# Optimization experiments

Hardware: AMD Instinct MI355X
Metric: run time of the kernel (lower is better)

The kernel has to match this reference:

```python
import jax, jax.numpy as jnp
import numpy as np

B, S, D, H = 2, 2048, 768, 12
E = D // H  # d_head = 64


def setup_inputs() -> dict:
    key = jax.random.key(0)
    ks = jax.random.split(key, 10)
    scale = 1.0 / np.sqrt(D)
    x = jax.random.normal(ks[0], (B, S, D), dtype=jnp.float32)
    # Additive mask, laid out [H*B, S, S] as the torch forward slices per head.
    attn_mask = jnp.zeros((H * B, S, S), dtype=jnp.float32)
    # Per-head projections (math form: q = x @ Wq[h] + bq[h])
    Wq = jax.random.normal(ks[1], (H, D, E), dtype=jnp.float32) * scale
    bq = jax.random.normal(ks[2], (H, E), dtype=jnp.float32) * 0.01
    Wk = jax.random.normal(ks[3], (H, D, E), dtype=jnp.float32) * scale
    bk = jax.random.normal(ks[4], (H, E), dtype=jnp.float32) * 0.01
    Wv = jax.random.normal(ks[5], (H, D, E), dtype=jnp.float32) * scale
    bv = jax.random.normal(ks[6], (H, E), dtype=jnp.float32) * 0.01
    Wo = jax.random.normal(ks[7], (D, D), dtype=jnp.float32) * scale
    bo = jax.random.normal(ks[8], (D,), dtype=jnp.float32) * 0.01
    return {"x": x, "attn_mask": attn_mask, "Wq": Wq, "bq": bq,
            "Wk": Wk, "bk": bk, "Wv": Wv, "bv": bv, "Wo": Wo, "bo": bo}


def reference(x, attn_mask, Wq, bq, Wk, bk, Wv, bv, Wo, bo):
    # x: [B,S,D]; attn_mask: [H*B,S,S]
    q = jnp.einsum('bsd,hde->hbse', x, Wq) + bq[:, None, None, :]
    k = jnp.einsum('bsd,hde->hbse', x, Wk) + bk[:, None, None, :]
    v = jnp.einsum('bsd,hde->hbse', x, Wv) + bv[:, None, None, :]
    mask = attn_mask.reshape(H, B, S, S)
    # NOTE: original code has NO 1/sqrt(d_head) scaling — kept faithful.
    logits = jnp.einsum('hbse,hbte->hbst', q, k) + mask
    w = jax.nn.softmax(logits, axis=-1)  # dropout is identity at eval / p=0
    o = jnp.einsum('hbst,hbte->hbse', w, v)  # [H,B,S,E]
    o = jnp.transpose(o, (1, 2, 0, 3)).reshape(B, S, H * E)  # concat heads
    return o @ Wo + bo
```

## Files before the change

kernel.cpp:

```cpp
#include <hip/hip_runtime.h>
#include <hip/hip_bf16.h>
#include <cmath>

constexpr int Bc  = 2;
constexpr int Sc  = 2048;
constexpr int Dc  = 768;
constexpr int Hc  = 12;
constexpr int Ec  = 64;
constexpr int BSc = Bc * Sc;

typedef _Float16 f16;
typedef __attribute__((ext_vector_type(8)))  _Float16 half8;
typedef __attribute__((ext_vector_type(16))) float    floatx16;

typedef __attribute__((address_space(3))) void       lds_void;
typedef __attribute__((address_space(1))) const void glb_cvoid;


__global__ __launch_bounds__(256) void prep_kernel(
    const float* __restrict__ x,
    const float* __restrict__ Wq, const float* __restrict__ Wk, const float* __restrict__ Wv,
    const float* __restrict__ bq, const float* __restrict__ bk, const float* __restrict__ bv,
    const float* __restrict__ Wo,
    f16* __restrict__ x16, f16* __restrict__ Wt16, f16* __restrict__ Wot16,
    float* __restrict__ bias_cat)
{
    __shared__ __align__(16) float Ts[64][65];
    const int t = threadIdx.x;
    int bid = blockIdx.x;

    if (bid < 1536) {
        const size_t base = (size_t)bid * 2048 + t * 8;
        const float4 v0 = *(const float4*)(x + base);
        const float4 v1 = *(const float4*)(x + base + 4);
        half8 hv;
        hv[0] = (f16)v0.x; hv[1] = (f16)v0.y; hv[2] = (f16)v0.z; hv[3] = (f16)v0.w;
        hv[4] = (f16)v1.x; hv[5] = (f16)v1.y; hv[6] = (f16)v1.z; hv[7] = (f16)v1.w;
        *(half8*)(x16 + base) = hv;
        return;
    }
    bid -= 1536;
    if (bid < 432) {
        const int proj = bid / 144, rem = bid % 144, h = rem / 12, dt = rem % 12;
        const float* W = ((proj == 0) ? Wq : (proj == 1) ? Wk : Wv) + (size_t)h * Dc * Ec;
        const int c = t & 63, rr = t >> 6;
        #pragma unroll
        for (int r0 = 0; r0 < 64; r0 += 4) {
            const int d = rr + r0;
            Ts[d][c] = W[(size_t)(dt * 64 + d) * Ec + c];
        }
        __syncthreads();
        #pragma unroll
        for (int r0 = 0; r0 < 64; r0 += 4) {
            const int e = rr + r0;
            Wt16[(size_t)(proj * 768 + h * 64 + e) * Dc + dt * 64 + c] = (f16)Ts[c][e];
        }
        return;
    }
    bid -= 432;
    if (bid < 144) {
        const int rt = bid / 12, ct = bid % 12;
        const int c = t & 63, rr = t >> 6;
        #pragma unroll
        for (int r0 = 0; r0 < 64; r0 += 4) {
            const int d = rr + r0;
            Ts[d][c] = Wo[(size_t)(rt * 64 + d) * Dc + ct * 64 + c];
        }
        __syncthreads();
        #pragma unroll
        for (int r0 = 0; r0 < 64; r0 += 4) {
            const int e = rr + r0;
            Wot16[(size_t)(ct * 64 + e) * Dc + rt * 64 + c] = (f16)Ts[c][e];
        }
        return;
    }
    bid -= 144;
    {
        const int g = bid * 256 + t;
        if (g < 3 * 768) {
            const int proj = g / 768, idx = g % 768;
            const float* bb = (proj == 0) ? bq : (proj == 1) ? bk : bv;
            bias_cat[g] = bb[idx];
        }
    }
}

__global__ __launch_bounds__(256, 2) void gemm_qkv_kernel(
    const f16* __restrict__ x16, const f16* __restrict__ Wt16,
    const float* __restrict__ bias_cat,
    f16* __restrict__ q16, f16* __restrict__ kswz, f16* __restrict__ vswz)
{
    __shared__ __align__(16) unsigned char smem[34816];
    f16 (*As)[64]  = (f16(*)[64])smem;
    f16 (*Bs)[64]  = (f16(*)[64])(smem + 16384);
    f16 (*Cs)[136] = (f16(*)[136])smem;

    const int t = threadIdx.x;
    const int wave = t >> 6, lane = t & 63;
    const int col = lane & 31, hf = lane >> 5;
    const int wr = wave & 1, wc = wave >> 1;
    const int m0 = blockIdx.x * 128, n0 = blockIdx.y * 128;
    const int lrow = lane >> 3, lseg = lane & 7;

    floatx16 c00, c01, c10, c11;
    #pragma unroll
    for (int i = 0; i < 16; ++i) { c00[i] = 0.f; c01[i] = 0.f; c10[i] = 0.f; c11[i] = 0.f; }

    for (int k0 = 0; k0 < Dc; k0 += 64) {
        #pragma unroll
        for (int i = 0; i < 4; ++i) {
            const int r = wave * 32 + i * 8;
            __builtin_amdgcn_global_load_lds(
                (glb_cvoid*)(x16 + (size_t)(m0 + r + lrow) * Dc + k0 + lseg * 8),
                (lds_void*)&As[r][0], 16, 0, 0);
            __builtin_amdgcn_global_load_lds(
                (glb_cvoid*)(Wt16 + (size_t)(n0 + r + lrow) * Dc + k0 + lseg * 8),
                (lds_void*)&Bs[r][0], 16, 0, 0);
        }
        __syncthreads();
        #pragma unroll
        for (int ks = 0; ks < 4; ++ks) {
            const half8 a0 = *(const half8*)&As[wr * 64 + col][ks * 16 + hf * 8];
            const half8 a1 = *(const half8*)&As[wr * 64 + 32 + col][ks * 16 + hf * 8];
            const half8 b0 = *(const half8*)&Bs[wc * 64 + col][ks * 16 + hf * 8];
            const half8 b1 = *(const half8*)&Bs[wc * 64 + 32 + col][ks * 16 + hf * 8];
            c00 = __builtin_amdgcn_mfma_f32_32x32x16_f16(a0, b0, c00, 0, 0, 0);
            c01 = __builtin_amdgcn_mfma_f32_32x32x16_f16(a0, b1, c01, 0, 0, 0);
            c10 = __builtin_amdgcn_mfma_f32_32x32x16_f16(a1, b0, c10, 0, 0, 0);
            c11 = __builtin_amdgcn_mfma_f32_32x32x16_f16(a1, b1, c11, 0, 0, 0);
        }
        __syncthreads();
    }

    const float bias0 = bias_cat[n0 + wc * 64 + col];
    const float bias1 = bias_cat[n0 + wc * 64 + 32 + col];
    #pragma unroll
    for (int i = 0; i < 16; ++i) {
        const int r = (i & 3) + 8 * (i >> 2) + 4 * hf;
        Cs[wr * 64 + r][wc * 64 + col]           = (f16)(c00[i] + bias0);
        Cs[wr * 64 + r][wc * 64 + 32 + col]      = (f16)(c01[i] + bias1);
        Cs[wr * 64 + 32 + r][wc * 64 + col]      = (f16)(c10[i] + bias0);
        Cs[wr * 64 + 32 + r][wc * 64 + 32 + col] = (f16)(c11[i] + bias1);
    }
    __syncthreads();

    const int proj = n0 / 768;
    const int h0   = (n0 - proj * 768) >> 6;
    const int b    = m0 >> 11;
    const int s_in = m0 & 2047;
    const int kt0  = s_in >> 5;

    if (proj == 0) {
        const int row = t >> 1, seg = t & 1;
        const int h = h0 + seg;
        f16* gp = q16 + ((size_t)(h * Bc + b) * Sc + s_in + row) * Ec;
        #pragma unroll
        for (int j = 0; j < 8; ++j)
            *(half8*)(gp + j * 8) = *(const half8*)&Cs[row][seg * 64 + j * 8];
    } else if (proj == 1) {
        #pragma unroll
        for (int ch = 0; ch < 8; ++ch) {
            const int id = ch * 256 + t;
            const int lane_ = id & 63;
            const int ks  = (id >> 6) & 3;
            const int ktp = (id >> 8) & 3;
            const int seg = (id >> 10) & 1;
            const int colp = lane_ & 31, hfp = lane_ >> 5;
            const int hb = (h0 + seg) * Bc + b;
            const half8 val = *(const half8*)&Cs[ktp * 32 + colp][seg * 64 + ks * 16 + hfp * 8];
            *(half8*)(kswz + ((size_t)((hb * 64 + kt0 + ktp) * 4 + ks) << 9) + lane_ * 8) = val;
        }
    } else {
        #pragma unroll
        for (int ch = 0; ch < 8; ++ch) {
            const int id = ch * 256 + t;
            const int lane_ = id & 63;
            const int ks2 = (id >> 6) & 1;
            const int vh  = (id >> 7) & 1;
            const int ktp = (id >> 8) & 3;
            const int seg = (id >> 10) & 1;
            const int colp = lane_ & 31, hfp = lane_ >> 5;
            const int hb = (h0 + seg) * Bc + b;
            const int e  = vh * 32 + colp;
            half8 val;
            #pragma unroll
            for (int j = 0; j < 8; ++j)
                val[j] = Cs[ktp * 32 + ks2 * 16 + hfp * 8 + j][seg * 64 + e];
            *(half8*)(vswz + ((size_t)(((hb * 64 + kt0 + ktp) * 2 + ks2) * 2 + vh) << 9) + lane_ * 8) = val;
        }
    }
}

__global__ __launch_bounds__(256, 2) void flash_attn_kernel(
    const f16* __restrict__ q16, const f16* __restrict__ kswz,
    const f16* __restrict__ vswz, const float* __restrict__ mask,
    f16* __restrict__ obuf16)
{
    __shared__ _Float16 Plds[4][32][40];
    __shared__ float Msh[2][2][32];
    __shared__ float Lsh[2][32];
    __shared__ float OLsh[2][64][33];

    const int rb   = blockIdx.x;
    const int b    = blockIdx.y;
    const int h    = blockIdx.z;
    const int hb   = h * Bc + b;
    const int t    = threadIdx.x;
    const int wave = t >> 6;
    const int lane = t & 63;
    const int rg   = wave & 1;
    const int kh   = wave >> 1;
    const int col  = lane & 31;
    const int hf   = lane >> 5;
    const int row0 = rb * 64 + rg * 32;

    const f16* qb  = q16  + ((size_t)hb * Sc + row0) * Ec;
    const f16* kbz = kswz + ((size_t)hb << 17);
    const f16* vbz = vswz + ((size_t)hb << 17);

    half8 qfrag[4];
    #pragma unroll
    for (int ks = 0; ks < 4; ++ks)
        qfrag[ks] = *(const half8*)(qb + (size_t)col * Ec + ks * 16 + hf * 8);

    constexpr int NT = (Sc / 2) / 32;

    float vmax[16];
    #pragma unroll
    for (int i = 0; i < 16; ++i) vmax[i] = -3e38f;

    half8 kreg[4];
    {
        const f16* kp = kbz + ((size_t)(kh * NT) << 11) + lane * 8;
        #pragma unroll
        for (int ks = 0; ks < 4; ++ks) kreg[ks] = *(const half8*)(kp + (ks << 9));
    }
    #pragma unroll 2
    for (int kt = 0; kt < NT; ++kt) {
        floatx16 c;
        #pragma unroll
        for (int i = 0; i < 16; ++i) c[i] = 0.f;
        #pragma unroll
        for (int ks = 0; ks < 4; ++ks)
            c = __builtin_amdgcn_mfma_f32_32x32x16_f16(qfrag[ks], kreg[ks], c, 0, 0, 0);
        if (kt + 1 < NT) {
            const f16* kp = kbz + ((size_t)(kh * NT + kt + 1) << 11) + lane * 8;
            #pragma unroll
            for (int ks = 0; ks < 4; ++ks) kreg[ks] = *(const half8*)(kp + (ks << 9));
        }
        #pragma unroll
        for (int i = 0; i < 16; ++i) vmax[i] = fmaxf(vmax[i], c[i]);
    }
    #pragma unroll
    for (int i = 0; i < 16; ++i) {
        float v = vmax[i];
        v = fmaxf(v, __shfl_xor(v, 1));
        v = fmaxf(v, __shfl_xor(v, 2));
        v = fmaxf(v, __shfl_xor(v, 4));
        v = fmaxf(v, __shfl_xor(v, 8));
        v = fmaxf(v, __shfl_xor(v, 16));
        vmax[i] = v;
    }
    if (col == 0) {
        #pragma unroll
        for (int i = 0; i < 16; ++i) {
            const int r = (i & 3) + 8 * (i >> 2) + 4 * hf;
            Msh[kh][rg][r] = vmax[i];
        }
    }
    __syncthreads();
    float mrow[16];
    #pragma unroll
    for (int i = 0; i < 16; ++i) {
        const int r = (i & 3) + 8 * (i >> 2) + 4 * hf;
        mrow[i] = fmaxf(vmax[i], Msh[1 - kh][rg][r]);
    }

    floatx16 o0, o1;
    float lsum[16];
    #pragma unroll
    for (int i = 0; i < 16; ++i) { o0[i] = 0.f; o1[i] = 0.f; lsum[i] = 0.f; }

    const float* mbase = mask + ((size_t)hb * Sc + row0) * Sc + col;
    const int key_base = kh * (Sc / 2);

    float mb[4][16];
    #pragma unroll
    for (int d = 0; d < 4; ++d)
        #pragma unroll
        for (int i = 0; i < 16; ++i) {
            const int r = (i & 3) + 8 * (i >> 2) + 4 * hf;
            mb[d][i] = __builtin_nontemporal_load(
                mbase + (size_t)r * Sc + key_base + d * 32);
        }
    {
        const f16* kp = kbz + ((size_t)(kh * NT) << 11) + lane * 8;
        #pragma unroll
        for (int ks = 0; ks < 4; ++ks) kreg[ks] = *(const half8*)(kp + (ks << 9));
    }

    for (int kt4 = 0; kt4 < NT; kt4 += 4) {
        #pragma unroll
        for (int s = 0; s < 4; ++s) {
            const int kt  = kt4 + s;
            const int ktg = kh * NT + kt;

            const f16* vp = vbz + ((size_t)ktg << 11) + lane * 8;
            const half8 va  = *(const half8*)(vp);
            const half8 vb0 = *(const half8*)(vp + (1 << 9));
            const half8 vc  = *(const half8*)(vp + (2 << 9));
            const half8 vd  = *(const half8*)(vp + (3 << 9));

            floatx16 c;
            #pragma unroll
            for (int i = 0; i < 16; ++i) c[i] = 0.f;
            #pragma unroll
            for (int ks = 0; ks < 4; ++ks)
                c = __builtin_amdgcn_mfma_f32_32x32x16_f16(qfrag[ks], kreg[ks], c, 0, 0, 0);

            if (kt + 1 < NT) {
                const f16* kp = kbz + ((size_t)(ktg + 1) << 11) + lane * 8;
                #pragma unroll
                for (int ks = 0; ks < 4; ++ks) kreg[ks] = *(const half8*)(kp + (ks << 9));
            }

            #pragma unroll
            for (int i = 0; i < 16; ++i) {
                const float p = __expf(c[i] + mb[s][i] - mrow[i]);
                lsum[i] += p;
                const int r = (i & 3) + 8 * (i >> 2) + 4 * hf;
                Plds[wave][r][col] = (f16)p;
            }
            if (kt4 + s + 4 < NT) {
                #pragma unroll
                for (int i = 0; i < 16; ++i) {
                    const int r = (i & 3) + 8 * (i >> 2) + 4 * hf;
                    mb[s][i] = __builtin_nontemporal_load(
                        mbase + (size_t)r * Sc + key_base + (kt + 4) * 32);
                }
            }
            asm volatile("s_waitcnt lgkmcnt(0)" ::: "memory");

            #pragma unroll
            for (int ks2 = 0; ks2 < 2; ++ks2) {
                const half8 pf = *(const half8*)(&Plds[wave][col][ks2 * 16 + hf * 8]);
                const half8 v0 = (ks2 == 0) ? va : vc;
                const half8 v1 = (ks2 == 0) ? vb0 : vd;
                o0 = __builtin_amdgcn_mfma_f32_32x32x16_f16(pf, v0, o0, 0, 0, 0);
                o1 = __builtin_amdgcn_mfma_f32_32x32x16_f16(pf, v1, o1, 0, 0, 0);
            }
        }
    }

    #pragma unroll
    for (int i = 0; i < 16; ++i) {
        float v = lsum[i];
        v += __shfl_xor(v, 1);
        v += __shfl_xor(v, 2);
        v += __shfl_xor(v, 4);
        v += __shfl_xor(v, 8);
        v += __shfl_xor(v, 16);
        lsum[i] = v;
    }

    if (kh == 1) {
        if (col == 0) {
            #pragma unroll
            for (int i = 0; i < 16; ++i) {
                const int r = (i & 3) + 8 * (i >> 2) + 4 * hf;
                Lsh[rg][r] = lsum[i];
            }
        }
        #pragma unroll
        for (int i = 0; i < 16; ++i) {
            OLsh[rg][lane][i]      = o0[i];
            OLsh[rg][lane][16 + i] = o1[i];
        }
    }
    __syncthreads();
    if (kh == 0) {
        #pragma unroll
        for (int i = 0; i < 16; ++i) {
            const int r = (i & 3) + 8 * (i >> 2) + 4 * hf;
            const float inv = 1.f / (lsum[i] + Lsh[rg][r]);
            const float r0 = (o0[i] + OLsh[rg][lane][i])      * inv;
            const float r1 = (o1[i] + OLsh[rg][lane][16 + i]) * inv;
            const size_t orow = ((size_t)b * Sc + row0 + r) * Dc + h * Ec;
            obuf16[orow + col]      = (f16)r0;
            obuf16[orow + 32 + col] = (f16)r1;
        }
    }
}

__global__ __launch_bounds__(256, 2) void gemm_out_kernel(
    const f16* __restrict__ a16, const f16* __restrict__ Wot16,
    const float* __restrict__ bo, float* __restrict__ out)
{
    __shared__ __align__(16) f16 As[128][64];
    __shared__ __align__(16) f16 Bs[64][64];

    const int t = threadIdx.x;
    const int wave = t >> 6, lane = t & 63;
    const int col = lane & 31, hf = lane >> 5;
    const int m0 = blockIdx.x * 128, n0 = blockIdx.y * 64;
    const int lrow = lane >> 3, lseg = lane & 7;

    floatx16 c0, c1;
    #pragma unroll
    for (int i = 0; i < 16; ++i) { c0[i] = 0.f; c1[i] = 0.f; }

    for (int k0 = 0; k0 < Dc; k0 += 64) {
        #pragma unroll
        for (int i = 0; i < 4; ++i) {
            const int r = wave * 32 + i * 8;
            __builtin_amdgcn_global_load_lds(
                (glb_cvoid*)(a16 + (size_t)(m0 + r + lrow) * Dc + k0 + lseg * 8),
                (lds_void*)&As[r][0], 16, 0, 0);
        }
        {
            const int r = wave * 16;
            __builtin_amdgcn_global_load_lds(
                (glb_cvoid*)(Wot16 + (size_t)(n0 + r + lrow) * Dc + k0 + lseg * 8),
                (lds_void*)&Bs[r][0], 16, 0, 0);
            __builtin_amdgcn_global_load_lds(
                (glb_cvoid*)(Wot16 + (size_t)(n0 + r + 8 + lrow) * Dc + k0 + lseg * 8),
                (lds_void*)&Bs[r + 8][0], 16, 0, 0);
        }
        __syncthreads();
        #pragma unroll
        for (int ks = 0; ks < 4; ++ks) {
            const half8 a  = *(const half8*)&As[wave * 32 + col][ks * 16 + hf * 8];
            const half8 b0 = *(const half8*)&Bs[col][ks * 16 + hf * 8];
            const half8 b1 = *(const half8*)&Bs[32 + col][ks * 16 + hf * 8];
            c0 = __builtin_amdgcn_mfma_f32_32x32x16_f16(a, b0, c0, 0, 0, 0);
            c1 = __builtin_amdgcn_mfma_f32_32x32x16_f16(a, b1, c1, 0, 0, 0);
        }
        __syncthreads();
    }

    const float bo0 = bo[n0 + col], bo1 = bo[n0 + 32 + col];
    #pragma unroll
    for (int i = 0; i < 16; ++i) {
        const int r = (i & 3) + 8 * (i >> 2) + 4 * hf;
        const size_t ro = (size_t)(m0 + wave * 32 + r) * Dc + n0;
        out[ro + col]      = c0[i] + bo0;
        out[ro + 32 + col] = c1[i] + bo1;
    }
}

extern "C" void kernel_launch(void* const* d_in, const int* in_sizes, int n_in,
                              void* d_out, int out_size, void* d_ws, size_t ws_size,
                              hipStream_t stream)
{
    const float* x    = (const float*)d_in[0];
    const float* mask = (const float*)d_in[1];
    const float* Wq   = (const float*)d_in[2];
    const float* bq   = (const float*)d_in[3];
    const float* Wk   = (const float*)d_in[4];
    const float* bk   = (const float*)d_in[5];
    const float* Wv   = (const float*)d_in[6];
    const float* bv   = (const float*)d_in[7];
    const float* Wo   = (const float*)d_in[8];
    const float* bo   = (const float*)d_in[9];
    float* out = (float*)d_out;

    constexpr size_t NQ = (size_t)Hc * Bc * Sc * Ec;
    f16* x16    = (f16*)d_ws;
    f16* Wt16   = x16 + (size_t)BSc * Dc;
    f16* Wot16  = Wt16 + (size_t)3 * Dc * Dc;
    f16* q16    = Wot16 + (size_t)Dc * Dc;
    f16* kswz   = q16 + NQ;
    f16* vswz   = kswz + NQ;
    f16* obuf16 = vswz + NQ;
    float* bias_cat = (float*)(obuf16 + NQ);

    prep_kernel<<<2121, 256, 0, stream>>>(x, Wq, Wk, Wv, bq, bk, bv, Wo,
                                          x16, Wt16, Wot16, bias_cat);

    gemm_qkv_kernel<<<dim3(BSc / 128, 2304 / 128), 256, 0, stream>>>(
        x16, Wt16, bias_cat, q16, kswz, vswz);

    flash_attn_kernel<<<dim3(Sc / 64, Bc, Hc), 256, 0, stream>>>(
        q16, kswz, vswz, mask, obuf16);

    gemm_out_kernel<<<dim3(BSc / 128, Dc / 64), 256, 0, stream>>>(
        obuf16, Wot16, bo, out);
}
```

Baseline: 677.9 us.

## Stage attention mask through LDS with coalesced float4 loads and remap block order

The mask is now read with row-coalesced float4 nontemporal loads, double-buffered in registers, and written to a per-wave LDS tile. The softmax reads it from that tile, replacing the previous scattered per-element global loads that were held in a large 64-float register array. Shared memory is overlaid into a single blob (mask tiles alias the output-reduction buffer), so a barrier is added before the reduction. The launch bound rises to 3 blocks per CU, and a 1D grid remaps blocks so that 8 head-batch pairs are interleaved. The cost is extra LDS traffic and tighter register limits.

```diff
diff --git a/kernel.cpp b/kernel.cpp
--- a/kernel.cpp
+++ b/kernel.cpp
@@ -12,6 +12,7 @@
 typedef _Float16 f16;
 typedef __attribute__((ext_vector_type(8)))  _Float16 half8;
 typedef __attribute__((ext_vector_type(16))) float    floatx16;
+typedef __attribute__((ext_vector_type(4)))  float    fx4;
 
 typedef __attribute__((address_space(3))) void       lds_void;
 typedef __attribute__((address_space(1))) const void glb_cvoid;
@@ -191,20 +192,25 @@
     }
 }
 
-__global__ __launch_bounds__(256, 2) void flash_attn_kernel(
+__global__ __launch_bounds__(256, 3) void flash_attn_kernel(
     const f16* __restrict__ q16, const f16* __restrict__ kswz,
     const f16* __restrict__ vswz, const float* __restrict__ mask,
     f16* __restrict__ obuf16)
 {
-    __shared__ _Float16 Plds[4][32][40];
-    __shared__ float Msh[2][2][32];
-    __shared__ float Lsh[2][32];
-    __shared__ float OLsh[2][64][33];
-
-    const int rb   = blockIdx.x;
-    const int b    = blockIdx.y;
-    const int h    = blockIdx.z;
-    const int hb   = h * Bc + b;
+    __shared__ __align__(16) unsigned char shblob[10240 + 16896 + 512 + 256];
+    _Float16 (*Plds)[32][40] = (_Float16(*)[32][40])shblob;
+    float*    Mall           = (float*)(shblob + 10240);
+    float    (*OLsh)[64][33] = (float(*)[64][33])(shblob + 10240);
+    float    (*Msh)[2][32]   = (float(*)[2][32])(shblob + 10240 + 16896);
+    float    (*Lsh)[32]      = (float(*)[32])(shblob + 10240 + 16896 + 512);
+
+    const int fblk = blockIdx.x;
+    const int kk   = fblk >> 3;
+    const int hb   = (fblk & 7) + 8 * (kk >> 5);
+    const int rb   = kk & 31;
+    const int h    = hb >> 1;
+    const int b    = hb & 1;
+
     const int t    = threadIdx.x;
     const int wave = t >> 6;
     const int lane = t & 63;
@@ -213,6 +219,8 @@
     const int col  = lane & 31;
     const int hf   = lane >> 5;
     const int row0 = rb * 64 + rg * 32;
+    const int lrow8 = lane >> 3;
+    const int lcol4 = (lane & 7) * 4;
 
     const f16* qb  = q16  + ((size_t)hb * Sc + row0) * Ec;
     const f16* kbz = kswz + ((size_t)hb << 17);
@@ -281,74 +289,78 @@
     #pragma unroll
     for (int i = 0; i < 16; ++i) { o0[i] = 0.f; o1[i] = 0.f; lsum[i] = 0.f; }
 
-    const float* mbase = mask + ((size_t)hb * Sc + row0) * Sc + col;
+    const float* mw = mask + ((size_t)hb * Sc + row0) * Sc;
     const int key_base = kh * (Sc / 2);
-
-    float mb[4][16];
-    #pragma unroll
-    for (int d = 0; d < 4; ++d)
+    float* Mw = Mall + wave * 1024;
+
+    fx4 mreg[4];
+    #pragma unroll
+    for (int j = 0; j < 4; ++j)
+        mreg[j] = __builtin_nontemporal_load(
+            (const fx4*)(mw + (size_t)(j * 8 + lrow8) * Sc + key_base + lcol4));
+    #pragma unroll
+    for (int j = 0; j < 4; ++j)
+        *(fx4*)&Mw[(j * 8 + lrow8) * 32 + lcol4] = mreg[j];
+    #pragma unroll
+    for (int j = 0; j < 4; ++j)
+        mreg[j] = __builtin_nontemporal_load(
+            (const fx4*)(mw + (size_t)(j * 8 + lrow8) * Sc + key_base + 32 + lcol4));
+    {
+        const f16* kp = kbz + ((size_t)(kh * NT) << 11) + lane * 8;
+        #pragma unroll
+        for (int ks = 0; ks < 4; ++ks) kreg[ks] = *(const half8*)(kp + (ks << 9));
+    }
+
+    for (int kt = 0; kt < NT; ++kt) {
+        const int ktg = kh * NT + kt;
+
+        const f16* vp = vbz + ((size_t)ktg << 11) + lane * 8;
+        const half8 va  = *(const half8*)(vp);
+        const half8 vb0 = *(const half8*)(vp + (1 << 9));
+        const half8 vc  = *(const half8*)(vp + (2 << 9));
+        const half8 vd  = *(const half8*)(vp + (3 << 9));
+
+        floatx16 c;
+        #pragma unroll
+        for (int i = 0; i < 16; ++i) c[i] = 0.f;
+        #pragma unroll
+        for (int ks = 0; ks < 4; ++ks)
+            c = __builtin_amdgcn_mfma_f32_32x32x16_f16(qfrag[ks], kreg[ks], c, 0, 0, 0);
+
+        if (kt + 1 < NT) {
+            const f16* kp = kbz + ((size_t)(ktg + 1) << 11) + lane * 8;
+            #pragma unroll
+            for (int ks = 0; ks < 4; ++ks) kreg[ks] = *(const half8*)(kp + (ks << 9));
+        }
+
         #pragma unroll
         for (int i = 0; i < 16; ++i) {
             const int r = (i & 3) + 8 * (i >> 2) + 4 * hf;
-            mb[d][i] = __builtin_nontemporal_load(
-                mbase + (size_t)r * Sc + key_base + d * 32);
-        }
-    {
-        const f16* kp = kbz + ((size_t)(kh * NT) << 11) + lane * 8;
-        #pragma unroll
-        for (int ks = 0; ks < 4; ++ks) kreg[ks] = *(const half8*)(kp + (ks << 9));
-    }
-
-    for (int kt4 = 0; kt4 < NT; kt4 += 4) {
-        #pragma unroll
-        for (int s = 0; s < 4; ++s) {
-            const int kt  = kt4 + s;
-            const int ktg = kh * NT + kt;
-
-            const f16* vp = vbz + ((size_t)ktg << 11) + lane * 8;
-            const half8 va  = *(const half8*)(vp);
-            const half8 vb0 = *(const half8*)(vp + (1 << 9));
-            const half8 vc  = *(const half8*)(vp + (2 << 9));
-            const half8 vd  = *(const half8*)(vp + (3 << 9));
-
-            floatx16 c;
+            const float p = __expf(c[i] + Mw[r * 32 + col] - mrow[i]);
+            lsum[i] += p;
+            Plds[wave][r][col] = (f16)p;
+        }
+        if (kt + 1 < NT) {
             #pragma unroll
-            for (int i = 0; i < 16; ++i) c[i] = 0.f;
+            for (int j = 0; j < 4; ++j)
+                *(fx4*)&Mw[(j * 8 + lrow8) * 32 + lcol4] = mreg[j];
+        }
+        if (kt + 2 < NT) {
             #pragma unroll
-            for (int ks = 0; ks < 4; ++ks)
-                c = __builtin_amdgcn_mfma_f32_32x32x16_f16(qfrag[ks], kreg[ks], c, 0, 0, 0);
-
-            if (kt + 1 < NT) {
-                const f16* kp = kbz + ((size_t)(ktg + 1) << 11) + lane * 8;
-                #pragma unroll
-                for (int ks = 0; ks < 4; ++ks) kreg[ks] = *(const half8*)(kp + (ks << 9));
-            }
-
-            #pragma unroll
-            for (int i = 0; i < 16; ++i) {
-                const float p = __expf(c[i] + mb[s][i] - mrow[i]);
-                lsum[i] += p;
-                const int r = (i & 3) + 8 * (i >> 2) + 4 * hf;
-                Plds[wave][r][col] = (f16)p;
-            }
-            if (kt4 + s + 4 < NT) {
-                #pragma unroll
-                for (int i = 0; i < 16; ++i) {
-                    const int r = (i & 3) + 8 * (i >> 2) + 4 * hf;
-                    mb[s][i] = __builtin_nontemporal_load(
-                        mbase + (size_t)r * Sc + key_base + (kt + 4) * 32);
-                }
-            }
-            asm volatile("s_waitcnt lgkmcnt(0)" ::: "memory");
-
-            #pragma unroll
-            for (int ks2 = 0; ks2 < 2; ++ks2) {
-                const half8 pf = *(const half8*)(&Plds[wave][col][ks2 * 16 + hf * 8]);
-                const half8 v0 = (ks2 == 0) ? va : vc;
-                const half8 v1 = (ks2 == 0) ? vb0 : vd;
-                o0 = __builtin_amdgcn_mfma_f32_32x32x16_f16(pf, v0, o0, 0, 0, 0);
-                o1 = __builtin_amdgcn_mfma_f32_32x32x16_f16(pf, v1, o1, 0, 0, 0);
-            }
+            for (int j = 0; j < 4; ++j)
+                mreg[j] = __builtin_nontemporal_load(
+                    (const fx4*)(mw + (size_t)(j * 8 + lrow8) * Sc
+                                 + key_base + (kt + 2) * 32 + lcol4));
+        }
+        asm volatile("s_waitcnt lgkmcnt(0)" ::: "memory");
+
+        #pragma unroll
+        for (int ks2 = 0; ks2 < 2; ++ks2) {
+            const half8 pf = *(const half8*)(&Plds[wave][col][ks2 * 16 + hf * 8]);
+            const half8 v0 = (ks2 == 0) ? va : vc;
+            const half8 v1 = (ks2 == 0) ? vb0 : vd;
+            o0 = __builtin_amdgcn_mfma_f32_32x32x16_f16(pf, v0, o0, 0, 0, 0);
+            o1 = __builtin_amdgcn_mfma_f32_32x32x16_f16(pf, v1, o1, 0, 0, 0);
         }
     }
 
@@ -363,6 +375,7 @@
         lsum[i] = v;
     }
 
+    __syncthreads();
     if (kh == 1) {
         if (col == 0) {
             #pragma unroll
@@ -480,7 +493,7 @@
     gemm_qkv_kernel<<<dim3(BSc / 128, 2304 / 128), 256, 0, stream>>>(
         x16, Wt16, bias_cat, q16, kswz, vswz);
 
-    flash_attn_kernel<<<dim3(Sc / 64, Bc, Hc), 256, 0, stream>>>(
+    flash_attn_kernel<<<768, 256, 0, stream>>>(
         q16, kswz, vswz, mask, obuf16);
 
     gemm_out_kernel<<<dim3(BSc / 128, Dc / 64), 256, 0, stream>>>(
```

Measured after the change: 665.3 us. No clear change (-1.9%).

## Stage mask tiles into LDS via async loads and drop key-split waves

Applied to the files above, without the earlier changes.

The attention kernel now uses 128-thread blocks of two waves. Each wave owns 32 query rows and loops over all keys, which removes the key-half split and its cross-wave max/sum/output merge through shared memory. The additive mask is now loaded per 64x128 band with global_load_lds directly into a 32KB LDS buffer, replacing the per-lane nontemporal register prefetch. A flattened grid remaps blocks so neighbouring blocks share heads. This lowers register pressure and coalesces the mask reads, but adds two barriers per round with no double-buffering, so mask load latency is exposed, and each wave now runs twice as many serial iterations.

```diff
diff --git a/kernel.cpp b/kernel.cpp
--- a/kernel.cpp
+++ b/kernel.cpp
@@ -191,39 +191,39 @@
     }
 }
 
-__global__ __launch_bounds__(256, 2) void flash_attn_kernel(
+__global__ __launch_bounds__(128, 2) void flash_attn_kernel(
     const f16* __restrict__ q16, const f16* __restrict__ kswz,
     const f16* __restrict__ vswz, const float* __restrict__ mask,
     f16* __restrict__ obuf16)
 {
-    __shared__ _Float16 Plds[4][32][40];
-    __shared__ float Msh[2][2][32];
-    __shared__ float Lsh[2][32];
-    __shared__ float OLsh[2][64][33];
-
-    const int rb   = blockIdx.x;
-    const int b    = blockIdx.y;
-    const int h    = blockIdx.z;
-    const int hb   = h * Bc + b;
+    __shared__ __align__(16) float Mall[64 * 128];
+    __shared__ _Float16 Plds[2][32][40];
+
+    const int fblk = blockIdx.x;
+    const int kk   = fblk >> 3;
+    const int hb   = (fblk & 7) + 8 * (kk >> 5);
+    const int rb   = kk & 31;
+    const int h    = hb >> 1;
+    const int b    = hb & 1;
+
     const int t    = threadIdx.x;
     const int wave = t >> 6;
     const int lane = t & 63;
-    const int rg   = wave & 1;
-    const int kh   = wave >> 1;
     const int col  = lane & 31;
     const int hf   = lane >> 5;
-    const int row0 = rb * 64 + rg * 32;
+    const int row0 = rb * 64 + wave * 32;
 
     const f16* qb  = q16  + ((size_t)hb * Sc + row0) * Ec;
     const f16* kbz = kswz + ((size_t)hb << 17);
     const f16* vbz = vswz + ((size_t)hb << 17);
+    const float* mband = mask + ((size_t)hb * Sc + rb * 64) * Sc;
 
     half8 qfrag[4];
     #pragma unroll
     for (int ks = 0; ks < 4; ++ks)
         qfrag[ks] = *(const half8*)(qb + (size_t)col * Ec + ks * 16 + hf * 8);
 
-    constexpr int NT = (Sc / 2) / 32;
+    constexpr int NT = Sc / 32;
 
     float vmax[16];
     #pragma unroll
@@ -231,7 +231,7 @@
 
     half8 kreg[4];
     {
-        const f16* kp = kbz + ((size_t)(kh * NT) << 11) + lane * 8;
+        const f16* kp = kbz + lane * 8;
         #pragma unroll
         for (int ks = 0; ks < 4; ++ks) kreg[ks] = *(const half8*)(kp + (ks << 9));
     }
@@ -244,13 +244,14 @@
         for (int ks = 0; ks < 4; ++ks)
             c = __builtin_amdgcn_mfma_f32_32x32x16_f16(qfrag[ks], kreg[ks], c, 0, 0, 0);
         if (kt + 1 < NT) {
-            const f16* kp = kbz + ((size_t)(kh * NT + kt + 1) << 11) + lane * 8;
+            const f16* kp = kbz + ((size_t)(kt + 1) << 11) + lane * 8;
             #pragma unroll
             for (int ks = 0; ks < 4; ++ks) kreg[ks] = *(const half8*)(kp + (ks << 9));
         }
         #pragma unroll
         for (int i = 0; i < 16; ++i) vmax[i] = fmaxf(vmax[i], c[i]);
     }
+    float mrow[16];
     #pragma unroll
     for (int i = 0; i < 16; ++i) {
         float v = vmax[i];
@@ -259,21 +260,7 @@
         v = fmaxf(v, __shfl_xor(v, 4));
         v = fmaxf(v, __shfl_xor(v, 8));
         v = fmaxf(v, __shfl_xor(v, 16));
-        vmax[i] = v;
-    }
-    if (col == 0) {
-        #pragma unroll
-        for (int i = 0; i < 16; ++i) {
-            const int r = (i & 3) + 8 * (i >> 2) + 4 * hf;
-            Msh[kh][rg][r] = vmax[i];
-        }
-    }
-    __syncthreads();
-    float mrow[16];
-    #pragma unroll
-    for (int i = 0; i < 16; ++i) {
-        const int r = (i & 3) + 8 * (i >> 2) + 4 * hf;
-        mrow[i] = fmaxf(vmax[i], Msh[1 - kh][rg][r]);
+        mrow[i] = v;
     }
 
     floatx16 o0, o1;
@@ -281,31 +268,29 @@
     #pragma unroll
     for (int i = 0; i < 16; ++i) { o0[i] = 0.f; o1[i] = 0.f; lsum[i] = 0.f; }
 
-    const float* mbase = mask + ((size_t)hb * Sc + row0) * Sc + col;
-    const int key_base = kh * (Sc / 2);
-
-    float mb[4][16];
-    #pragma unroll
-    for (int d = 0; d < 4; ++d)
-        #pragma unroll
-        for (int i = 0; i < 16; ++i) {
-            const int r = (i & 3) + 8 * (i >> 2) + 4 * hf;
-            mb[d][i] = __builtin_nontemporal_load(
-                mbase + (size_t)r * Sc + key_base + d * 32);
-        }
     {
-        const f16* kp = kbz + ((size_t)(kh * NT) << 11) + lane * 8;
+        const f16* kp = kbz + lane * 8;
         #pragma unroll
         for (int ks = 0; ks < 4; ++ks) kreg[ks] = *(const half8*)(kp + (ks << 9));
     }
 
-    for (int kt4 = 0; kt4 < NT; kt4 += 4) {
+    for (int rd = 0; rd < NT / 4; ++rd) {
+        __syncthreads();
+        #pragma unroll
+        for (int j = 0; j < 16; ++j) {
+            const int row = wave * 32 + 2 * j;
+            __builtin_amdgcn_global_load_lds(
+                (glb_cvoid*)(mband + (size_t)(row + (lane >> 5)) * Sc
+                             + rd * 128 + (lane & 31) * 4),
+                (lds_void*)&Mall[row * 128], 16, 0, 0);
+        }
+        __syncthreads();
+
         #pragma unroll
         for (int s = 0; s < 4; ++s) {
-            const int kt  = kt4 + s;
-            const int ktg = kh * NT + kt;
-
-            const f16* vp = vbz + ((size_t)ktg << 11) + lane * 8;
+            const int kt = rd * 4 + s;
+
+            const f16* vp = vbz + ((size_t)kt << 11) + lane * 8;
             const half8 va  = *(const half8*)(vp);
             const half8 vb0 = *(const half8*)(vp + (1 << 9));
             const half8 vc  = *(const half8*)(vp + (2 << 9));
@@ -319,25 +304,18 @@
                 c = __builtin_amdgcn_mfma_f32_32x32x16_f16(qfrag[ks], kreg[ks], c, 0, 0, 0);
 
             if (kt + 1 < NT) {
-                const f16* kp = kbz + ((size_t)(ktg + 1) << 11) + lane * 8;
+                const f16* kp = kbz + ((size_t)(kt + 1) << 11) + lane * 8;
                 #pragma unroll
                 for (int ks = 0; ks < 4; ++ks) kreg[ks] = *(const half8*)(kp + (ks << 9));
             }
 
             #pragma unroll
             for (int i = 0; i < 16; ++i) {
-                const float p = __expf(c[i] + mb[s][i] - mrow[i]);
+                const int r = (i & 3) + 8 * (i >> 2) + 4 * hf;
+                const float m = Mall[(wave * 32 + r) * 128 + s * 32 + col];
+                const float p = __expf(c[i] + m - mrow[i]);
                 lsum[i] += p;
-                const int r = (i & 3) + 8 * (i >> 2) + 4 * hf;
                 Plds[wave][r][col] = (f16)p;
-            }
-            if (kt4 + s + 4 < NT) {
-                #pragma unroll
-                for (int i = 0; i < 16; ++i) {
-                    const int r = (i & 3) + 8 * (i >> 2) + 4 * hf;
-                    mb[s][i] = __builtin_nontemporal_load(
-                        mbase + (size_t)r * Sc + key_base + (kt + 4) * 32);
-                }
             }
             asm volatile("s_waitcnt lgkmcnt(0)" ::: "memory");
 
@@ -360,35 +338,11 @@
         v += __shfl_xor(v, 4);
         v += __shfl_xor(v, 8);
         v += __shfl_xor(v, 16);
-        lsum[i] = v;
-    }
-
-    if (kh == 1) {
-        if (col == 0) {
-            #pragma unroll
-            for (int i = 0; i < 16; ++i) {
-                const int r = (i & 3) + 8 * (i >> 2) + 4 * hf;
-                Lsh[rg][r] = lsum[i];
-            }
-        }
-        #pragma unroll
-        for (int i = 0; i < 16; ++i) {
-            OLsh[rg][lane][i]      = o0[i];
-            OLsh[rg][lane][16 + i] = o1[i];
-        }
-    }
-    __syncthreads();
-    if (kh == 0) {
-        #pragma unroll
-        for (int i = 0; i < 16; ++i) {
-            const int r = (i & 3) + 8 * (i >> 2) + 4 * hf;
-            const float inv = 1.f / (lsum[i] + Lsh[rg][r]);
-            const float r0 = (o0[i] + OLsh[rg][lane][i])      * inv;
-            const float r1 = (o1[i] + OLsh[rg][lane][16 + i]) * inv;
-            const size_t orow = ((size_t)b * Sc + row0 + r) * Dc + h * Ec;
-            obuf16[orow + col]      = (f16)r0;
-            obuf16[orow + 32 + col] = (f16)r1;
-        }
+        const float inv = 1.f / v;
+        const int r = (i & 3) + 8 * (i >> 2) + 4 * hf;
+        const size_t orow = ((size_t)b * Sc + row0 + r) * Dc + h * Ec;
+        obuf16[orow + col]      = (f16)(o0[i] * inv);
+        obuf16[orow + 32 + col] = (f16)(o1[i] * inv);
     }
 }
 
@@ -480,7 +434,7 @@
     gemm_qkv_kernel<<<dim3(BSc / 128, 2304 / 128), 256, 0, stream>>>(
         x16, Wt16, bias_cat, q16, kswz, vswz);
 
-    flash_attn_kernel<<<dim3(Sc / 64, Bc, Hc), 256, 0, stream>>>(
+    flash_attn_kernel<<<768, 128, 0, stream>>>(
         q16, kswz, vswz, mask, obuf16);
 
     gemm_out_kernel<<<dim3(BSc / 128, Dc / 64), 256, 0, stream>>>(
```

Result: faster. 642.8 us (-5.2%).
